# Kernel tuning notes

Hardware: AMD Instinct MI355X
Metric: run time of the kernel (lower is better)

Reference implementation:

```python
import jax, jax.numpy as jnp
import numpy as np

NT, NS, NH, NG, NR, NC = 365, 300, 128, 32, 8, 1


def _linear_params(key, fin, fout):
    k1, k2 = jax.random.split(key)
    s = 1.0 / np.sqrt(fin)
    W = jax.random.uniform(k1, (fout, fin), minval=-s, maxval=s, dtype=jnp.float32)
    b = jax.random.uniform(k2, (fout,), minval=-s, maxval=s, dtype=jnp.float32)
    return W, b


def setup_inputs() -> dict:
    key = jax.random.key(0)
    ks = jax.random.split(key, 9)
    x = jax.random.normal(ks[0], (NT, NS, 6), dtype=jnp.float32)
    xc = jax.random.normal(ks[1], (NS, NG), dtype=jnp.float32)
    fcR_w1, fcR_b1 = _linear_params(ks[2], NG, 256)
    fcR_w2, fcR_b2 = _linear_params(ks[3], 256, NH * NR)
    fcW_w1, fcW_b1 = _linear_params(ks[4], NG, 256)
    fcW_w2, fcW_b2 = _linear_params(ks[5], 256, NH * 7)
    fcT_w1, fcT_b1 = _linear_params(ks[6], 6 + NG, 256)
    fcT_w2, fcT_b2 = _linear_params(ks[7], 256, NH * 3)
    fcCT_w, fcCT_b = _linear_params(ks[8], 2 + NG, NC * NH * 3)
    return dict(x=x, xc=xc,
                fcR_w1=fcR_w1, fcR_b1=fcR_b1, fcR_w2=fcR_w2, fcR_b2=fcR_b2,
                fcW_w1=fcW_w1, fcW_b1=fcW_b1, fcW_w2=fcW_w2, fcW_b2=fcW_b2,
                fcT_w1=fcT_w1, fcT_b1=fcT_b1, fcT_w2=fcT_w2, fcT_b2=fcT_b2,
                fcCT_w=fcCT_w, fcCT_b=fcCT_b)


def _mlp(x, w1, b1, w2, b2):
    # Linear -> Tanh -> Dropout(identity in eval) -> Linear
    h = jnp.tanh(x @ w1.T + b1)
    return h @ w2.T + b2


def _conv_ts(q, r):
    # q: [nt, ns, nh]; r: [ns, nh, nr] routing weights. Causal temporal conv:
    # out[t] = sum_i q[t-i] * r[..., i]  (zero padded on the left)
    nt = q.shape[0]
    nr = r.shape[-1]
    qp = jnp.concatenate([jnp.zeros((nr - 1,) + q.shape[1:], q.dtype), q], axis=0)
    out = qp[nr - 1: nr - 1 + nt] * r[None, :, :, 0]
    for i in range(1, nr):
        out = out + qp[nr - 1 - i: nr - 1 - i + nt] * r[None, :, :, i]
    return out


def reference(x, xc, fcR_w1, fcR_b1, fcR_w2, fcR_b2,
              fcW_w1, fcW_b1, fcW_w2, fcW_b2,
              fcT_w1, fcT_b1, fcT_w2, fcT_b2,
              fcCT_w, fcCT_b):
    nh, nr = NH, NR
    P, E, T1, T2 = x[..., 0], x[..., 1], x[..., 2], x[..., 3]
    nt, ns = P.shape
    xcT = jnp.broadcast_to(xc[None], (nt, ns, xc.shape[-1]))
    xT = jnp.concatenate([x, xcT], axis=-1)                      # [nt, ns, 6+ng]

    # static gates per (site, bucket): sepPar with ['sigmoid']*4,'exp','relu','skip'
    w = _mlp(xc, fcW_w1, fcW_b1, fcW_w2, fcW_b2)                 # [ns, nh*7]
    kp = jax.nn.sigmoid(w[:, 0 * nh:1 * nh])
    ks_ = jax.nn.sigmoid(w[:, 1 * nh:2 * nh])
    kg = jax.nn.sigmoid(w[:, 2 * nh:3 * nh])
    gp = jax.nn.sigmoid(w[:, 3 * nh:4 * nh])
    gL = jnp.exp(w[:, 4 * nh:5 * nh]) * 2.0
    qb = jax.nn.relu(w[:, 5 * nh:6 * nh])
    ga = jax.nn.softmax(w[:, 6 * nh:7 * nh], axis=1)             # [ns, nh]

    # time-varying gates: ['skip','relu','exp']; vi overridden by hardsigmoid(v*2)
    v = _mlp(xT, fcT_w1, fcT_b1, fcT_w2, fcT_b2)                 # [nt, ns, nh*3]
    vi = jnp.clip(v[:, :, :nh] * 2.0 / 6.0 + 0.5, 0.0, 1.0)     # F.hardsigmoid(v*2)
    ve = jax.nn.relu(v[:, :, nh:2 * nh]) * 2.0
    vm = jnp.exp(v[:, :, 2 * nh:3 * nh])

    wR = _mlp(xc, fcR_w1, fcR_b1, fcR_w2, fcR_b2)                # [ns, nh*nr]
    r = jax.nn.relu(wR[:, :nh * nr]).reshape(ns, nh, nr)

    # snow fraction vf = arccos((T1+T2)/(T2-T1))/3.1415, overridden at extremes
    denom = T2 - T1
    ratio = jnp.clip((T1 + T2) / jnp.where(denom == 0, 1.0, denom), -1.0, 1.0)
    vf = jnp.arccos(ratio) / 3.1415
    vf = jnp.where(T1 >= 0, 0.0, jnp.where(T2 <= 0, 1.0, vf))
    Ps = P * vf                                                  # snow  [nt, ns]
    Pl = (P * (1.0 - vf))[:, :, None] * vi                       # rain  [nt, ns, nh]
    Ev = E[:, :, None] * ve                                      # evap  [nt, ns, nh]

    def step(carry, inp):
        Sf, Ss, Sg = carry
        Ps_k, Pl_k, Ev_k, vm_k = inp
        qf = jnp.minimum(Sf + Ps_k, vm_k)
        Sf = jax.nn.relu(Sf + Ps_k - vm_k)
        H = jax.nn.relu(Ss + Pl_k + qf - Ev_k)
        qp_ = jax.nn.relu(kp * (H - gL))
        qs = ks_ * jnp.minimum(H, gL)
        Ss = H - qp_ - qs
        qso = qs * (1.0 - gp)
        qsg = qs * gp
        qg = kg * (Sg + qsg) + qb
        Sg = (1.0 - kg) * (Sg + qsg) - qb
        return (Sf, Ss, Sg), (qp_, qso, qg)

    z = jnp.zeros((ns, nh), dtype=x.dtype)
    _, (Q1T, Q2T, Q3T) = jax.lax.scan(step, (z, z, z),
                                      (Ps[:, :, None], Pl, Ev, vm))

    Q1R = _conv_ts(Q1T, r)
    Q2R = _conv_ts(Q2T, r)
    Q3R = _conv_ts(Q3T, r)
    outQ = jnp.sum((Q1R + Q2R + Q3R) * ga, axis=2)               # [nt, ns]

    xTc = jnp.concatenate([T1[:, :, None], T2[:, :, None], xcT], axis=-1)
    wC = xTc @ fcCT_w.T + fcCT_b                                 # [nt, ns, nh*3]
    cp = jnp.exp(wC[:, :, 0 * nh:1 * nh])
    cs = jnp.exp(wC[:, :, 1 * nh:2 * nh])
    cg = jnp.exp(wC[:, :, 2 * nh:3 * nh])
    C1R = _conv_ts(Q1T * cp / 10.0, r)
    C2R = _conv_ts(Q2T * cs, r)
    C3R = _conv_ts(Q3T * cg, r)
    outC = jnp.sum((C1R + C2R + C3R) * ga, axis=2) / outQ
    return outQ, outC
```

## Files before the change

### kernel.cpp

```cpp
#include <hip/hip_runtime.h>
#include <math.h>

#define NTT 365
#define NSS 300
#define NROWS (NTT*NSS)
#define TPAD2 416

using bf16x8 = __attribute__((ext_vector_type(8))) short;
using f32x4  = __attribute__((ext_vector_type(4))) float;

__device__ __forceinline__ float sigf(float v) { return 1.0f / (1.0f + __expf(-v)); }

__device__ __forceinline__ float tanhfast(float x) {
    float e = __expf(2.0f * x);
    return 1.0f - 2.0f * __builtin_amdgcn_rcpf(1.0f + e);
}

__device__ __forceinline__ unsigned short f2bf(float f) {
    unsigned u = __builtin_bit_cast(unsigned, f);
    u += 0x7FFFu + ((u >> 16) & 1u);
    return (unsigned short)(u >> 16);
}

__global__ __launch_bounds__(256) void k_prep(const float* __restrict__ w1,
                                              const float* __restrict__ w2,
                                              unsigned short* __restrict__ w1s,
                                              unsigned short* __restrict__ w2s)
{
    int G = blockIdx.x * 256 + threadIdx.x;
    if (G < 2048) {
        int lane = G & 63, ks = (G >> 6) & 1, tile = G >> 7;
        int o = tile * 16 + (lane & 15);
        int kb = ks * 32 + (lane >> 4) * 8;
        unsigned short tmp[8];
#pragma unroll
        for (int e = 0; e < 8; ++e) {
            int k = kb + e;
            tmp[e] = (k < 38) ? f2bf(w1[o * 38 + k]) : (unsigned short)0;
        }
        *(bf16x8*)(w1s + (size_t)G * 8) = *(bf16x8*)tmp;
    } else if (G < 2048 + 12288) {
        int G2 = G - 2048;
        int lane = G2 & 63, ks = (G2 >> 6) & 7, tile = G2 >> 9;
        int o = tile * 16 + (lane & 15);
        int kb = ks * 32 + (lane >> 4) * 8;
        unsigned short tmp[8];
#pragma unroll
        for (int e = 0; e < 8; ++e) tmp[e] = f2bf(w2[o * 256 + kb + e]);
        *(bf16x8*)(w2s + (size_t)G2 * 8) = *(bf16x8*)tmp;
    }
}

__global__ __launch_bounds__(256) void k_site(
    const float* __restrict__ xc,
    const float* __restrict__ wW1, const float* __restrict__ bW1,
    const float* __restrict__ wW2, const float* __restrict__ bW2,
    const float* __restrict__ wR1, const float* __restrict__ bR1,
    const float* __restrict__ wR2, const float* __restrict__ bR2,
    float* __restrict__ wsite, float* __restrict__ rsite)
{
    __shared__ float xcb[10][32];
    __shared__ float hW[10][256];
    __shared__ float hR[10][256];
    int tid = threadIdx.x;
    int s0 = blockIdx.x * 10;
    int os = blockIdx.y;
    for (int i = tid; i < 10 * 32; i += 256) xcb[i / 32][i % 32] = xc[s0 * 32 + i];
    __syncthreads();
    {
        int j = tid;
        float aW[10], aR[10];
#pragma unroll
        for (int r = 0; r < 10; ++r) { aW[r] = bW1[j]; aR[r] = bR1[j]; }
        for (int k = 0; k < 32; ++k) {
            float wv = wW1[j * 32 + k], rv = wR1[j * 32 + k];
#pragma unroll
            for (int r = 0; r < 10; ++r) { float xv = xcb[r][k]; aW[r] += xv * wv; aR[r] += xv * rv; }
        }
#pragma unroll
        for (int r = 0; r < 10; ++r) { hW[r][j] = tanhfast(aW[r]); hR[r][j] = tanhfast(aR[r]); }
    }
    __syncthreads();
    if (tid < 240) {
        int o_lin = os * 240 + tid;
        float acc[10];
        if (o_lin < 896) {
            int o = o_lin;
#pragma unroll
            for (int r = 0; r < 10; ++r) acc[r] = bW2[o];
            for (int k = 0; k < 256; ++k) {
                float wv = wW2[o * 256 + k];
#pragma unroll
                for (int r = 0; r < 10; ++r) acc[r] += hW[r][k] * wv;
            }
#pragma unroll
            for (int r = 0; r < 10; ++r) wsite[(s0 + r) * 896 + o] = acc[r];
        } else {
            int o = o_lin - 896;
#pragma unroll
            for (int r = 0; r < 10; ++r) acc[r] = bR2[o];
            for (int k = 0; k < 256; ++k) {
                float wv = wR2[o * 256 + k];
#pragma unroll
                for (int r = 0; r < 10; ++r) acc[r] += hR[r][k] * wv;
            }
#pragma unroll
            for (int r = 0; r < 10; ++r) rsite[(s0 + r) * 1024 + o] = acc[r];
        }
    }
}

__global__ __launch_bounds__(128) void k_softmax_ga(const float* __restrict__ wsite,
                                                    float* __restrict__ ga)
{
    int s = blockIdx.x, tid = threadIdx.x;
    __shared__ float red[2];
    float v = wsite[s * 896 + 6 * 128 + tid];
    float m = v;
#pragma unroll
    for (int off = 32; off >= 1; off >>= 1) m = fmaxf(m, __shfl_xor(m, off));
    if ((tid & 63) == 0) red[tid >> 6] = m;
    __syncthreads();
    m = fmaxf(red[0], red[1]);
    __syncthreads();
    float e = __expf(v - m);
    float ssum = e;
#pragma unroll
    for (int off = 32; off >= 1; off >>= 1) ssum += __shfl_xor(ssum, off);
    if ((tid & 63) == 0) red[tid >> 6] = ssum;
    __syncthreads();
    ssum = red[0] + red[1];
    ga[s * 128 + tid] = e / ssum;
}

__global__ __launch_bounds__(128) void k_ct(const float* __restrict__ xc,
                                            const float* __restrict__ ctw,
                                            const float* __restrict__ ctb,
                                            float* __restrict__ ctp8,
                                            float* __restrict__ ctpb)
{
    __shared__ float xcs[32];
    int s = blockIdx.x, h = threadIdx.x;
    if (h < 32) xcs[h] = xc[s * 32 + h];
    __syncthreads();
    const float L2E = 1.4426950408889634f;
    const float LG01 = -3.3219280948873623f;
    float out[8];
    float cgb = 0.0f;
#pragma unroll
    for (int g = 0; g < 3; ++g) {
        const float* wr = ctw + (g * 128 + h) * 34;
        float base = ctb[g * 128 + h];
        for (int k = 0; k < 32; ++k) base += wr[2 + k] * xcs[k];
        float w0 = wr[0] * L2E, w1 = wr[1] * L2E;
        float bb = base * L2E + ((g == 0) ? LG01 : 0.0f);
        if (g == 0) { out[0] = w0; out[1] = w1; out[2] = bb; }
        else if (g == 1) { out[3] = w0; out[4] = w1; out[5] = bb; }
        else { out[6] = w0; out[7] = w1; cgb = bb; }
    }
    float4* dst = (float4*)(ctp8 + ((size_t)s * 128 + h) * 8);
    dst[0] = make_float4(out[0], out[1], out[2], out[3]);
    dst[1] = make_float4(out[4], out[5], out[6], out[7]);
    ctpb[(size_t)s * 128 + h] = cgb;
}

__global__ __launch_bounds__(512, 4) void k_fcT(
    const float* __restrict__ x, const float* __restrict__ xc,
    const unsigned short* __restrict__ w1s, const float* __restrict__ b1,
    const unsigned short* __restrict__ w2s, const float* __restrict__ b2,
    float4* __restrict__ PTt, unsigned* __restrict__ NVu)
{
    __shared__ unsigned short A1[64][72];
    __shared__ unsigned short hb[64][264];
    __shared__ float2 pfE[64];
    int tid = threadIdx.x;
    int row0 = blockIdx.x * 64;

    for (int idx = tid; idx < 64 * 64; idx += 512) {
        int r = idx >> 6, c = idx & 63;
        int g = row0 + r;
        float val = 0.0f;
        if (g < NROWS) {
            if (c < 6) val = x[g * 6 + c];
            else if (c < 38) { int s = g % NSS; val = xc[s * 32 + (c - 6)]; }
        }
        A1[r][c] = f2bf(val);
    }
    if (tid < 64) {
        int r = tid, g = row0 + r;
        float P = 0, E = 0, T1 = 0, T2 = 0;
        if (g < NROWS) { P = x[g * 6]; E = x[g * 6 + 1]; T1 = x[g * 6 + 2]; T2 = x[g * 6 + 3]; }
        float den = T2 - T1;
        float dg = (den == 0.0f) ? 1.0f : den;
        float ratio = fminf(fmaxf((T1 + T2) / dg, -1.0f), 1.0f);
        float vf = acosf(ratio) * (1.0f / 3.1415f);
        vf = (T1 >= 0.0f) ? 0.0f : ((T2 <= 0.0f) ? 1.0f : vf);
        pfE[r] = make_float2(P * (1.0f - vf), 2.0f * E);
        if (g < NROWS) {
            int tg = g / NSS, sg = g - tg * NSS;
            PTt[(size_t)sg * TPAD2 + tg] = make_float4(P * vf, T1, T2, vf);
        }
    }
    __syncthreads();

    int lane = tid & 63, wv = tid >> 6;
    int r16 = lane & 15;
    int kg = (lane >> 4) * 8;
    int rq = (lane >> 4) * 4;

    {
        int mt = wv & 3, nb = (wv >> 2) * 8;
        f32x4 acc[8];
#pragma unroll
        for (int i = 0; i < 8; ++i) acc[i] = (f32x4){0.f, 0.f, 0.f, 0.f};
#pragma unroll
        for (int ks = 0; ks < 2; ++ks) {
            bf16x8 a = *(const bf16x8*)&A1[mt * 16 + r16][ks * 32 + kg];
#pragma unroll
            for (int i = 0; i < 8; ++i) {
                bf16x8 b = *(const bf16x8*)(w1s + ((size_t)(((nb + i) * 2 + ks) * 64 + lane) << 3));
                acc[i] = __builtin_amdgcn_mfma_f32_16x16x32_bf16(a, b, acc[i], 0, 0, 0);
            }
        }
#pragma unroll
        for (int i = 0; i < 8; ++i) {
            int col = (nb + i) * 16 + r16;
            float bias = b1[col];
#pragma unroll
            for (int j = 0; j < 4; ++j) {
                int row = mt * 16 + rq + j;
                hb[row][col] = f2bf(tanhfast(acc[i][j] + bias));
            }
        }
    }
    __syncthreads();

    {
        int t0 = wv, t1 = wv + 8, t2 = wv + 16;
        f32x4 acc[4][3];
#pragma unroll
        for (int m = 0; m < 4; ++m)
#pragma unroll
            for (int c = 0; c < 3; ++c) acc[m][c] = (f32x4){0.f, 0.f, 0.f, 0.f};
#pragma unroll
        for (int ks = 0; ks < 8; ++ks) {
            bf16x8 b0 = *(const bf16x8*)(w2s + ((size_t)((t0 * 8 + ks) * 64 + lane) << 3));
            bf16x8 b1v = *(const bf16x8*)(w2s + ((size_t)((t1 * 8 + ks) * 64 + lane) << 3));
            bf16x8 b2v = *(const bf16x8*)(w2s + ((size_t)((t2 * 8 + ks) * 64 + lane) << 3));
#pragma unroll
            for (int m = 0; m < 4; ++m) {
                bf16x8 a = *(const bf16x8*)&hb[m * 16 + r16][ks * 32 + kg];
                acc[m][0] = __builtin_amdgcn_mfma_f32_16x16x32_bf16(a, b0, acc[m][0], 0, 0, 0);
                acc[m][1] = __builtin_amdgcn_mfma_f32_16x16x32_bf16(a, b1v, acc[m][1], 0, 0, 0);
                acc[m][2] = __builtin_amdgcn_mfma_f32_16x16x32_bf16(a, b2v, acc[m][2], 0, 0, 0);
            }
        }
        int hcol = wv * 16 + r16;
        float bias0 = b2[hcol], bias1 = b2[128 + hcol], bias2 = b2[256 + hcol];
#pragma unroll
        for (int m = 0; m < 4; ++m) {
            float2 pf[4];
#pragma unroll
            for (int j = 0; j < 4; ++j) pf[j] = pfE[m * 16 + rq + j];
#pragma unroll
            for (int j = 0; j < 4; ++j) {
                int r = m * 16 + rq + j;
                int g = row0 + r;
                if (g < NROWS) {
                    float vi = fminf(fmaxf((acc[m][0][j] + bias0) * (1.0f / 3.0f) + 0.5f, 0.0f), 1.0f);
                    float pl = pf[j].x * vi;
                    float ev = pf[j].y * fmaxf(acc[m][1][j] + bias1, 0.0f);
                    float vmv = __expf(acc[m][2][j] + bias2);
                    unsigned pk = (unsigned)f2bf(pl - ev) | ((unsigned)f2bf(vmv) << 16);
                    int tg = g / NSS, sg = g - tg * NSS;
                    NVu[((size_t)sg * TPAD2 + tg) * 128 + hcol] = pk;
                }
            }
        }
    }
}

template<int ISC>
__device__ __forceinline__ void scan_loop(
    int lane, int s, int half,
    float kp, float ks, float kg, float gp, float gpc, float gL, float kpgl, float qb,
    float r0, float r1, float r2, float r3, float r4, float r5, float r6, float r7,
    float cpw0, float cpw1, float cpb, float csw0, float csw1, float csb,
    float cgw0, float cgw1, float cgb,
    const unsigned* __restrict__ nvsite, const float4* ptlds, float (*red)[68],
    float* __restrict__ outp)
{
    float Sf = 0.0f, Ss = 0.0f, Sg = 0.0f;
    float a0 = 0, a1 = 0, a2 = 0, a3 = 0, a4 = 0, a5 = 0, a6 = 0, a7 = 0;
    unsigned A[16], B[16];
    float4 pt[4];
#pragma unroll
    for (int i = 0; i < 16; ++i) A[i] = nvsite[(size_t)i * 128];
#pragma unroll
    for (int i = 0; i < 4; ++i) pt[i] = ptlds[i];

    auto STEP = [&](int t, int uu, unsigned nvu, unsigned& pref) {
        pref = nvsite[(size_t)(t + 16) * 128];
        float net = __builtin_bit_cast(float, nvu << 16);
        float vm  = __builtin_bit_cast(float, nvu & 0xFFFF0000u);
        int ps = uu & 3;
        float psv = pt[ps].x, T1 = pt[ps].y, T2 = pt[ps].z;
        pt[ps] = ptlds[t + 4];
        float t1v = Sf + psv;
        float qf = fminf(t1v, vm);
        Sf = fmaxf(t1v - vm, 0.0f);
        float H = fmaxf(Ss + qf + net, 0.0f);
        float qp = fmaxf(kp * H - kpgl, 0.0f);
        float qs = ks * fminf(H, gL);
        Ss = H - qp - qs;
        float qso = qs * gpc;
        float qsg = qs * gp;
        float tg2 = Sg + qsg;
        float qg = kg * tg2 + qb;
        Sg = tg2 - qg;
        float val;
        if (ISC) {
            float cp = exp2f(cpw0 * T1 + cpw1 * T2 + cpb);
            float cs = exp2f(csw0 * T1 + csw1 * T2 + csb);
            float cg = exp2f(cgw0 * T1 + cgw1 * T2 + cgb);
            val = qp * cp + qso * cs + qg * cg;
        } else {
            val = qp + qso + qg;
        }
        a0 += val * r0; a1 += val * r1; a2 += val * r2; a3 += val * r3;
        a4 += val * r4; a5 += val * r5; a6 += val * r6; a7 += val * r7;
        red[uu & 15][lane] = a0;
        a0 = a1; a1 = a2; a2 = a3; a3 = a4; a4 = a5; a5 = a6; a6 = a7; a7 = 0.0f;
    };

    auto RED = [&](int base) {
        int v = lane >> 2, sub = lane & 3;
        const float4* rp4 = (const float4*)&red[v][0];
        float4 x0 = rp4[sub * 4 + 0];
        float4 x1 = rp4[sub * 4 + 1];
        float4 x2 = rp4[sub * 4 + 2];
        float4 x3 = rp4[sub * 4 + 3];
        float sA = (x0.x + x0.y) + (x0.z + x0.w);
        float sB = (x1.x + x1.y) + (x1.z + x1.w);
        float sC = (x2.x + x2.y) + (x2.z + x2.w);
        float sD = (x3.x + x3.y) + (x3.z + x3.w);
        float sm = (sA + sB) + (sC + sD);
        sm += __shfl_xor(sm, 1);
        sm += __shfl_xor(sm, 2);
        int tt = base + v;
        if (sub == 0 && tt < NTT)
            outp[((size_t)tt * NSS + s) * 2 + half] = sm;
    };

    for (int tb = 0; tb < 384; tb += 32) {
#pragma unroll
        for (int u = 0; u < 16; ++u) STEP(tb + u, u, A[u], B[u]);
        RED(tb);
#pragma unroll
        for (int u = 0; u < 16; ++u) STEP(tb + 16 + u, u + 16, B[u], A[u]);
        RED(tb + 16);
    }
}

__global__ __launch_bounds__(64, 2) void k_scan(
    const float* __restrict__ wsite, const float* __restrict__ rsite,
    const float* __restrict__ gaw,
    const float* __restrict__ ctp8, const float* __restrict__ ctpb,
    const float4* __restrict__ PTt, const unsigned* __restrict__ NVu,
    float* __restrict__ pQ, float* __restrict__ pC)
{
    __shared__ float4 ptlds[TPAD2];
    __shared__ __align__(16) float red[16][68];
    int lane = threadIdx.x;
    int b = blockIdx.x;
    int s = (b >> 5) * 8 + (b & 7);
    int hr = (b >> 3) & 3;
    int half = hr >> 1, role = hr & 1;
    if (s >= NSS) return;
    int h = half * 64 + lane;

    for (int t = lane; t < TPAD2; t += 64) ptlds[t] = PTt[(size_t)s * TPAD2 + t];

    const float* wrow = wsite + s * 896;
    float kp = sigf(wrow[0 * 128 + h]);
    float ks = sigf(wrow[1 * 128 + h]);
    float kg = sigf(wrow[2 * 128 + h]);
    float gp = sigf(wrow[3 * 128 + h]);
    float gpc = 1.0f - gp;
    float gL = __expf(wrow[4 * 128 + h]) * 2.0f;
    float kpgl = kp * gL;
    float qb = fmaxf(wrow[5 * 128 + h], 0.0f);
    float ga = gaw[s * 128 + h];
    float4 rrA = *(const float4*)(rsite + s * 1024 + h * 8);
    float4 rrB = *(const float4*)(rsite + s * 1024 + h * 8 + 4);
    float r0 = fmaxf(rrA.x, 0.0f) * ga;
    float r1 = fmaxf(rrA.y, 0.0f) * ga;
    float r2 = fmaxf(rrA.z, 0.0f) * ga;
    float r3 = fmaxf(rrA.w, 0.0f) * ga;
    float r4 = fmaxf(rrB.x, 0.0f) * ga;
    float r5 = fmaxf(rrB.y, 0.0f) * ga;
    float r6 = fmaxf(rrB.z, 0.0f) * ga;
    float r7 = fmaxf(rrB.w, 0.0f) * ga;

    const unsigned* nvsite = NVu + (size_t)s * TPAD2 * 128 + h;

    if (role == 0) {
        scan_loop<0>(lane, s, half, kp, ks, kg, gp, gpc, gL, kpgl, qb,
                     r0, r1, r2, r3, r4, r5, r6, r7,
                     0.f, 0.f, 0.f, 0.f, 0.f, 0.f, 0.f, 0.f, 0.f,
                     nvsite, ptlds, red, pQ);
    } else {
        const float4* cp4 = (const float4*)(ctp8 + ((size_t)s * 128 + h) * 8);
        float4 c0 = cp4[0], c1 = cp4[1];
        float cgb = ctpb[(size_t)s * 128 + h];
        scan_loop<1>(lane, s, half, kp, ks, kg, gp, gpc, gL, kpgl, qb,
                     r0, r1, r2, r3, r4, r5, r6, r7,
                     c0.x, c0.y, c0.z, c0.w, c1.x, c1.y, c1.z, c1.w, cgb,
                     nvsite, ptlds, red, pC);
    }
}

__global__ __launch_bounds__(256) void k_final(const float* __restrict__ pQ,
                                               const float* __restrict__ pC,
                                               float* __restrict__ out)
{
    int i = blockIdx.x * 256 + threadIdx.x;
    if (i < NROWS) {
        float q = pQ[i * 2] + pQ[i * 2 + 1];
        float c = pC[i * 2] + pC[i * 2 + 1];
        out[i] = q;
        out[NROWS + i] = c / q;
    }
}

extern "C" void kernel_launch(void* const* d_in, const int* in_sizes, int n_in,
                              void* d_out, int out_size, void* d_ws, size_t ws_size,
                              hipStream_t stream)
{
    const float* x      = (const float*)d_in[0];
    const float* xc     = (const float*)d_in[1];
    const float* fcR_w1 = (const float*)d_in[2];
    const float* fcR_b1 = (const float*)d_in[3];
    const float* fcR_w2 = (const float*)d_in[4];
    const float* fcR_b2 = (const float*)d_in[5];
    const float* fcW_w1 = (const float*)d_in[6];
    const float* fcW_b1 = (const float*)d_in[7];
    const float* fcW_w2 = (const float*)d_in[8];
    const float* fcW_b2 = (const float*)d_in[9];
    const float* fcT_w1 = (const float*)d_in[10];
    const float* fcT_b1 = (const float*)d_in[11];
    const float* fcT_w2 = (const float*)d_in[12];
    const float* fcT_b2 = (const float*)d_in[13];
    const float* fcCT_w = (const float*)d_in[14];
    const float* fcCT_b = (const float*)d_in[15];
    float* out = (float*)d_out;

    float* ws = (float*)d_ws;
    size_t o_w    = 0;
    size_t o_r    = o_w  + 300 * 896;
    size_t o_ga   = o_r  + 300 * 1024;
    size_t o_PT   = o_ga + 300 * 128;
    size_t o_NV   = o_PT + (size_t)TPAD2 * NSS * 4;
    size_t o_pQ   = o_NV + (size_t)TPAD2 * NSS * 128;
    size_t o_pC   = o_pQ + (size_t)NROWS * 2;
    size_t o_w1bf = o_pC + (size_t)NROWS * 2;
    size_t o_w2bf = o_w1bf + 8192;
    size_t o_ctp  = o_w2bf + 49152;
    size_t o_ctpb = o_ctp + (size_t)300 * 128 * 8;

    float* wsite = ws + o_w;
    float* rsite = ws + o_r;
    float* gaw   = ws + o_ga;
    float4* PTt  = (float4*)(ws + o_PT);
    unsigned* NVu = (unsigned*)(ws + o_NV);
    float* pQ    = ws + o_pQ;
    float* pC    = ws + o_pC;
    unsigned short* w1s = (unsigned short*)(ws + o_w1bf);
    unsigned short* w2s = (unsigned short*)(ws + o_w2bf);
    float* ctp8  = ws + o_ctp;
    float* ctpb  = ws + o_ctpb;

    k_prep<<<56, 256, 0, stream>>>(fcT_w1, fcT_w2, w1s, w2s);
    k_site<<<dim3(30, 8), 256, 0, stream>>>(xc, fcW_w1, fcW_b1, fcW_w2, fcW_b2,
                                            fcR_w1, fcR_b1, fcR_w2, fcR_b2, wsite, rsite);
    k_softmax_ga<<<300, 128, 0, stream>>>(wsite, gaw);
    k_ct<<<300, 128, 0, stream>>>(xc, fcCT_w, fcCT_b, ctp8, ctpb);
    int nblk2 = (NROWS + 63) / 64;
    k_fcT<<<nblk2, 512, 0, stream>>>(x, xc, w1s, fcT_b1, w2s, fcT_b2, PTt, NVu);
    k_scan<<<1216, 64, 0, stream>>>(wsite, rsite, gaw, ctp8, ctpb,
                                    PTt, NVu, pQ, pC);
    k_final<<<(NROWS + 255) / 256, 256, 0, stream>>>(pQ, pC, out);
}
```

Measured before the change: 174.4 us.

## Process two hidden units per scan thread and store NV in time-major order

Each scan thread now handles two adjacent hidden units, so one 64-lane block covers all 128 units of a site. This halves the number of scan blocks and removes the split partial outputs and their combine in the final kernel. The NV buffer is now written in natural row order (time-major), which drops the per-element divide in the fcT epilogue and lets the scan fetch two units per load with uint2. The trade-off is fewer waves in flight for the latency-bound serial scan, offset by two independent recurrences per thread for more instruction-level parallelism. Prefetch rows past the end of the sequence read uninitialised padding, but those rows only feed outputs that are discarded.

Result: slower. 192.5 us (+10.4%).

```diff
diff --git a/kernel.cpp b/kernel.cpp
--- a/kernel.cpp
+++ b/kernel.cpp
@@ -5,6 +5,7 @@
 #define NSS 300
 #define NROWS (NTT*NSS)
 #define TPAD2 416
+#define NVROWS 384
 
 using bf16x8 = __attribute__((ext_vector_type(8))) short;
 using f32x4  = __attribute__((ext_vector_type(4))) float;
@@ -272,8 +273,7 @@
                     float ev = pf[j].y * fmaxf(acc[m][1][j] + bias1, 0.0f);
                     float vmv = __expf(acc[m][2][j] + bias2);
                     unsigned pk = (unsigned)f2bf(pl - ev) | ((unsigned)f2bf(vmv) << 16);
-                    int tg = g / NSS, sg = g - tg * NSS;
-                    NVu[((size_t)sg * TPAD2 + tg) * 128 + hcol] = pk;
+                    NVu[(size_t)g * 128 + hcol] = pk;
                 }
             }
         }
@@ -281,56 +281,123 @@
 }
 
 template<int ISC>
-__device__ __forceinline__ void scan_loop(
-    int lane, int s, int half,
-    float kp, float ks, float kg, float gp, float gpc, float gL, float kpgl, float qb,
-    float r0, float r1, float r2, float r3, float r4, float r5, float r6, float r7,
-    float cpw0, float cpw1, float cpb, float csw0, float csw1, float csb,
-    float cgw0, float cgw1, float cgb,
-    const unsigned* __restrict__ nvsite, const float4* ptlds, float (*red)[68],
+__device__ __forceinline__ void scan_body(
+    int lane, int s,
+    const float* __restrict__ wrow, const float* __restrict__ rsite,
+    const float* __restrict__ gaw, const float* __restrict__ ctp8,
+    const float* __restrict__ ctpb,
+    const unsigned* __restrict__ NVu, const float4* ptlds, float (*red)[68],
     float* __restrict__ outp)
 {
-    float Sf = 0.0f, Ss = 0.0f, Sg = 0.0f;
+    float kp[2], ksv[2], kgv[2], gpv[2], gpc[2], gLv[2], kpgl[2], qbv[2];
+    {
+        float2 v0 = *(const float2*)(wrow + 0 * 128 + 2 * lane);
+        float2 v1 = *(const float2*)(wrow + 1 * 128 + 2 * lane);
+        float2 v2 = *(const float2*)(wrow + 2 * 128 + 2 * lane);
+        float2 v3 = *(const float2*)(wrow + 3 * 128 + 2 * lane);
+        float2 v4 = *(const float2*)(wrow + 4 * 128 + 2 * lane);
+        float2 v5 = *(const float2*)(wrow + 5 * 128 + 2 * lane);
+        kp[0] = sigf(v0.x); kp[1] = sigf(v0.y);
+        ksv[0] = sigf(v1.x); ksv[1] = sigf(v1.y);
+        kgv[0] = sigf(v2.x); kgv[1] = sigf(v2.y);
+        gpv[0] = sigf(v3.x); gpv[1] = sigf(v3.y);
+        gpc[0] = 1.0f - gpv[0]; gpc[1] = 1.0f - gpv[1];
+        gLv[0] = __expf(v4.x) * 2.0f; gLv[1] = __expf(v4.y) * 2.0f;
+        kpgl[0] = kp[0] * gLv[0]; kpgl[1] = kp[1] * gLv[1];
+        qbv[0] = fmaxf(v5.x, 0.0f); qbv[1] = fmaxf(v5.y, 0.0f);
+    }
+    float2 gav = *(const float2*)(gaw + s * 128 + 2 * lane);
+    float r[2][8];
+#pragma unroll
+    for (int c = 0; c < 2; ++c) {
+        float ga = (c == 0) ? gav.x : gav.y;
+        float4 ra = *(const float4*)(rsite + s * 1024 + (2 * lane + c) * 8);
+        float4 rb = *(const float4*)(rsite + s * 1024 + (2 * lane + c) * 8 + 4);
+        r[c][0] = fmaxf(ra.x, 0.f) * ga; r[c][1] = fmaxf(ra.y, 0.f) * ga;
+        r[c][2] = fmaxf(ra.z, 0.f) * ga; r[c][3] = fmaxf(ra.w, 0.f) * ga;
+        r[c][4] = fmaxf(rb.x, 0.f) * ga; r[c][5] = fmaxf(rb.y, 0.f) * ga;
+        r[c][6] = fmaxf(rb.z, 0.f) * ga; r[c][7] = fmaxf(rb.w, 0.f) * ga;
+    }
+    float ct[2][9];
+    if (ISC) {
+#pragma unroll
+        for (int c = 0; c < 2; ++c) {
+            const float4* cp4 = (const float4*)(ctp8 + ((size_t)s * 128 + 2 * lane + c) * 8);
+            float4 c0 = cp4[0], c1 = cp4[1];
+            ct[c][0] = c0.x; ct[c][1] = c0.y; ct[c][2] = c0.z;
+            ct[c][3] = c0.w; ct[c][4] = c1.x; ct[c][5] = c1.y;
+            ct[c][6] = c1.z; ct[c][7] = c1.w;
+            ct[c][8] = ctpb[(size_t)s * 128 + 2 * lane + c];
+        }
+    }
+
+    float Sf[2] = {0.f, 0.f}, Ss[2] = {0.f, 0.f}, Sg[2] = {0.f, 0.f};
     float a0 = 0, a1 = 0, a2 = 0, a3 = 0, a4 = 0, a5 = 0, a6 = 0, a7 = 0;
-    unsigned A[16], B[16];
+
+    const unsigned* nvrow = NVu + (size_t)s * 128 + 2 * lane;
+#define NVLD(t) (*(const uint2*)(nvrow + (size_t)(t) * (NSS * 128)))
+
+    uint2 A[8], B[8];
+#pragma unroll
+    for (int i = 0; i < 8; ++i) A[i] = NVLD(i);
+#pragma unroll
+    for (int i = 0; i < 8; ++i) B[i] = NVLD(8 + i);
     float4 pt[4];
 #pragma unroll
-    for (int i = 0; i < 16; ++i) A[i] = nvsite[(size_t)i * 128];
-#pragma unroll
     for (int i = 0; i < 4; ++i) pt[i] = ptlds[i];
 
-    auto STEP = [&](int t, int uu, unsigned nvu, unsigned& pref) {
-        pref = nvsite[(size_t)(t + 16) * 128];
-        float net = __builtin_bit_cast(float, nvu << 16);
-        float vm  = __builtin_bit_cast(float, nvu & 0xFFFF0000u);
-        int ps = uu & 3;
+    auto STEP = [&](int t, uint2 nv) {
+        int ps = t & 3;
         float psv = pt[ps].x, T1 = pt[ps].y, T2 = pt[ps].z;
         pt[ps] = ptlds[t + 4];
-        float t1v = Sf + psv;
-        float qf = fminf(t1v, vm);
-        Sf = fmaxf(t1v - vm, 0.0f);
-        float H = fmaxf(Ss + qf + net, 0.0f);
-        float qp = fmaxf(kp * H - kpgl, 0.0f);
-        float qs = ks * fminf(H, gL);
-        Ss = H - qp - qs;
-        float qso = qs * gpc;
-        float qsg = qs * gp;
-        float tg2 = Sg + qsg;
-        float qg = kg * tg2 + qb;
-        Sg = tg2 - qg;
-        float val;
-        if (ISC) {
-            float cp = exp2f(cpw0 * T1 + cpw1 * T2 + cpb);
-            float cs = exp2f(csw0 * T1 + csw1 * T2 + csb);
-            float cg = exp2f(cgw0 * T1 + cgw1 * T2 + cgb);
-            val = qp * cp + qso * cs + qg * cg;
-        } else {
-            val = qp + qso + qg;
-        }
-        a0 += val * r0; a1 += val * r1; a2 += val * r2; a3 += val * r3;
-        a4 += val * r4; a5 += val * r5; a6 += val * r6; a7 += val * r7;
-        red[uu & 15][lane] = a0;
+        unsigned nvw[2] = {nv.x, nv.y};
+        float val[2];
+#pragma unroll
+        for (int c = 0; c < 2; ++c) {
+            float net = __builtin_bit_cast(float, nvw[c] << 16);
+            float vm  = __builtin_bit_cast(float, nvw[c] & 0xFFFF0000u);
+            float t1v = Sf[c] + psv;
+            float qf = fminf(t1v, vm);
+            Sf[c] = fmaxf(t1v - vm, 0.0f);
+            float H = fmaxf(Ss[c] + qf + net, 0.0f);
+            float qp = fmaxf(kp[c] * H - kpgl[c], 0.0f);
+            float qs = ksv[c] * fminf(H, gLv[c]);
+            Ss[c] = H - qp - qs;
+            float qso = qs * gpc[c];
+            float qsg = qs * gpv[c];
+            float tg2 = Sg[c] + qsg;
+            float qg = kgv[c] * tg2 + qbv[c];
+            Sg[c] = tg2 - qg;
+            if (ISC) {
+                float cp = exp2f(ct[c][0] * T1 + ct[c][1] * T2 + ct[c][2]);
+                float cs = exp2f(ct[c][3] * T1 + ct[c][4] * T2 + ct[c][5]);
+                float cg = exp2f(ct[c][6] * T1 + ct[c][7] * T2 + ct[c][8]);
+                val[c] = qp * cp + qso * cs + qg * cg;
+            } else {
+                val[c] = qp + qso + qg;
+            }
+        }
+        a0 += val[0] * r[0][0]; a0 += val[1] * r[1][0];
+        a1 += val[0] * r[0][1]; a1 += val[1] * r[1][1];
+        a2 += val[0] * r[0][2]; a2 += val[1] * r[1][2];
+        a3 += val[0] * r[0][3]; a3 += val[1] * r[1][3];
+        a4 += val[0] * r[0][4]; a4 += val[1] * r[1][4];
+        a5 += val[0] * r[0][5]; a5 += val[1] * r[1][5];
+        a6 += val[0] * r[0][6]; a6 += val[1] * r[1][6];
+        a7 += val[0] * r[0][7]; a7 += val[1] * r[1][7];
+        red[t & 15][lane] = a0;
         a0 = a1; a1 = a2; a2 = a3; a3 = a4; a4 = a5; a5 = a6; a6 = a7; a7 = 0.0f;
+    };
+
+    auto GROUP = [&](int tb, uint2 (&BUF)[8]) {
+#pragma unroll
+        for (int u = 0; u < 8; ++u) {
+            int t = tb + u;
+            uint2 cur = BUF[u];
+            BUF[u] = NVLD(t + 16);
+            STEP(t, cur);
+        }
+        asm volatile("" ::: "memory");
     };
 
     auto RED = [&](int base) {
@@ -348,21 +415,19 @@
         sm += __shfl_xor(sm, 1);
         sm += __shfl_xor(sm, 2);
         int tt = base + v;
-        if (sub == 0 && tt < NTT)
-            outp[((size_t)tt * NSS + s) * 2 + half] = sm;
+        if (sub == 0 && tt < NTT) outp[(size_t)tt * NSS + s] = sm;
     };
 
-    for (int tb = 0; tb < 384; tb += 32) {
-#pragma unroll
-        for (int u = 0; u < 16; ++u) STEP(tb + u, u, A[u], B[u]);
+    for (int tb = 0; tb < 368; tb += 16) {
+        GROUP(tb, A);
+        GROUP(tb + 8, B);
         RED(tb);
-#pragma unroll
-        for (int u = 0; u < 16; ++u) STEP(tb + 16 + u, u + 16, B[u], A[u]);
-        RED(tb + 16);
-    }
-}
-
-__global__ __launch_bounds__(64, 2) void k_scan(
+    }
+#undef NVLD
+}
+
+__global__ __launch_bounds__(64) __attribute__((amdgpu_waves_per_eu(1, 2)))
+void k_scan(
     const float* __restrict__ wsite, const float* __restrict__ rsite,
     const float* __restrict__ gaw,
     const float* __restrict__ ctp8, const float* __restrict__ ctpb,
@@ -373,51 +438,18 @@
     __shared__ __align__(16) float red[16][68];
     int lane = threadIdx.x;
     int b = blockIdx.x;
-    int s = (b >> 5) * 8 + (b & 7);
-    int hr = (b >> 3) & 3;
-    int half = hr >> 1, role = hr & 1;
+    int lo = b & 7, q = b >> 3;
+    int s = (q >> 1) * 8 + lo;
+    int role = q & 1;
     if (s >= NSS) return;
-    int h = half * 64 + lane;
 
     for (int t = lane; t < TPAD2; t += 64) ptlds[t] = PTt[(size_t)s * TPAD2 + t];
 
     const float* wrow = wsite + s * 896;
-    float kp = sigf(wrow[0 * 128 + h]);
-    float ks = sigf(wrow[1 * 128 + h]);
-    float kg = sigf(wrow[2 * 128 + h]);
-    float gp = sigf(wrow[3 * 128 + h]);
-    float gpc = 1.0f - gp;
-    float gL = __expf(wrow[4 * 128 + h]) * 2.0f;
-    float kpgl = kp * gL;
-    float qb = fmaxf(wrow[5 * 128 + h], 0.0f);
-    float ga = gaw[s * 128 + h];
-    float4 rrA = *(const float4*)(rsite + s * 1024 + h * 8);
-    float4 rrB = *(const float4*)(rsite + s * 1024 + h * 8 + 4);
-    float r0 = fmaxf(rrA.x, 0.0f) * ga;
-    float r1 = fmaxf(rrA.y, 0.0f) * ga;
-    float r2 = fmaxf(rrA.z, 0.0f) * ga;
-    float r3 = fmaxf(rrA.w, 0.0f) * ga;
-    float r4 = fmaxf(rrB.x, 0.0f) * ga;
-    float r5 = fmaxf(rrB.y, 0.0f) * ga;
-    float r6 = fmaxf(rrB.z, 0.0f) * ga;
-    float r7 = fmaxf(rrB.w, 0.0f) * ga;
-
-    const unsigned* nvsite = NVu + (size_t)s * TPAD2 * 128 + h;
-
-    if (role == 0) {
-        scan_loop<0>(lane, s, half, kp, ks, kg, gp, gpc, gL, kpgl, qb,
-                     r0, r1, r2, r3, r4, r5, r6, r7,
-                     0.f, 0.f, 0.f, 0.f, 0.f, 0.f, 0.f, 0.f, 0.f,
-                     nvsite, ptlds, red, pQ);
-    } else {
-        const float4* cp4 = (const float4*)(ctp8 + ((size_t)s * 128 + h) * 8);
-        float4 c0 = cp4[0], c1 = cp4[1];
-        float cgb = ctpb[(size_t)s * 128 + h];
-        scan_loop<1>(lane, s, half, kp, ks, kg, gp, gpc, gL, kpgl, qb,
-                     r0, r1, r2, r3, r4, r5, r6, r7,
-                     c0.x, c0.y, c0.z, c0.w, c1.x, c1.y, c1.z, c1.w, cgb,
-                     nvsite, ptlds, red, pC);
-    }
+    if (role == 0)
+        scan_body<0>(lane, s, wrow, rsite, gaw, ctp8, ctpb, NVu, ptlds, red, pQ);
+    else
+        scan_body<1>(lane, s, wrow, rsite, gaw, ctp8, ctpb, NVu, ptlds, red, pC);
 }
 
 __global__ __launch_bounds__(256) void k_final(const float* __restrict__ pQ,
@@ -426,10 +458,9 @@
 {
     int i = blockIdx.x * 256 + threadIdx.x;
     if (i < NROWS) {
-        float q = pQ[i * 2] + pQ[i * 2 + 1];
-        float c = pC[i * 2] + pC[i * 2 + 1];
+        float q = pQ[i];
         out[i] = q;
-        out[NROWS + i] = c / q;
+        out[NROWS + i] = pC[i] / q;
     }
 }
 
@@ -461,9 +492,9 @@
     size_t o_ga   = o_r  + 300 * 1024;
     size_t o_PT   = o_ga + 300 * 128;
     size_t o_NV   = o_PT + (size_t)TPAD2 * NSS * 4;
-    size_t o_pQ   = o_NV + (size_t)TPAD2 * NSS * 128;
-    size_t o_pC   = o_pQ + (size_t)NROWS * 2;
-    size_t o_w1bf = o_pC + (size_t)NROWS * 2;
+    size_t o_pQ   = o_NV + (size_t)NVROWS * NSS * 128;
+    size_t o_pC   = o_pQ + (size_t)NROWS;
+    size_t o_w1bf = o_pC + (size_t)NROWS;
     size_t o_w2bf = o_w1bf + 8192;
     size_t o_ctp  = o_w2bf + 49152;
     size_t o_ctpb = o_ctp + (size_t)300 * 128 * 8;
@@ -487,7 +518,7 @@
     k_ct<<<300, 128, 0, stream>>>(xc, fcCT_w, fcCT_b, ctp8, ctpb);
     int nblk2 = (NROWS + 63) / 64;
     k_fcT<<<nblk2, 512, 0, stream>>>(x, xc, w1s, fcT_b1, w2s, fcT_b2, PTt, NVu);
-    k_scan<<<1216, 64, 0, stream>>>(wsite, rsite, gaw, ctp8, ctpb,
-                                    PTt, NVu, pQ, pC);
+    k_scan<<<608, 64, 0, stream>>>(wsite, rsite, gaw, ctp8, ctpb,
+                                   PTt, NVu, pQ, pC);
     k_final<<<(NROWS + 255) / 256, 256, 0, stream>>>(pQ, pC, out);
 }
```
